# Kernel optimization log

Hardware: AMD Instinct MI355X
Metric: run time of the kernel (lower is better)

## Reference

```python
import jax, jax.numpy as jnp
import numpy as np

LEAKY_SLOPE = 0.2  # tf.nn.leaky_relu default alpha
N_NODES = 50000
N_EDGES = 800000
IN_DIM = 128
OUT_DIM = 64
HEADS = 4
MLP_HID = 256
MLP_OUT = 128


def setup_inputs() -> dict:
    key = jax.random.key(0)
    ks = jax.random.split(key, 10)
    node_embeddings = jax.random.normal(ks[0], (N_NODES, IN_DIM), dtype=jnp.float32)
    src = jax.random.randint(ks[1], (N_EDGES,), 0, N_NODES, dtype=jnp.int32)
    dst = jax.random.randint(ks[2], (N_EDGES,), 0, N_NODES, dtype=jnp.int32)
    # glorot-ish scales
    W_n = jax.random.normal(ks[3], (HEADS, IN_DIM, OUT_DIM), dtype=jnp.float32) * (1.0 / np.sqrt(IN_DIM))
    a_src = jax.random.normal(ks[4], (HEADS, OUT_DIM), dtype=jnp.float32) * (1.0 / np.sqrt(OUT_DIM))
    a_dst = jax.random.normal(ks[5], (HEADS, OUT_DIM), dtype=jnp.float32) * (1.0 / np.sqrt(OUT_DIM))
    mlp_W1 = jax.random.normal(ks[6], (HEADS * OUT_DIM, MLP_HID), dtype=jnp.float32) * (1.0 / np.sqrt(HEADS * OUT_DIM))
    mlp_b1 = jnp.zeros((MLP_HID,), dtype=jnp.float32)
    mlp_W2 = jax.random.normal(ks[7], (MLP_HID, MLP_OUT), dtype=jnp.float32) * (1.0 / np.sqrt(MLP_HID))
    mlp_b2 = jnp.zeros((MLP_OUT,), dtype=jnp.float32)
    return {"node_embeddings": node_embeddings, "src": src, "dst": dst,
            "W_n": W_n, "a_src": a_src, "a_dst": a_dst,
            "mlp_W1": mlp_W1, "mlp_b1": mlp_b1, "mlp_W2": mlp_W2, "mlp_b2": mlp_b2}


def _gat_forward(node_embeddings, src, dst, W_n, a_src, a_dst, mlp_W1, mlp_b1, mlp_W2, mlp_b2):
    N = node_embeddings.shape[0]
    # per-head linear transform: [N, H, D]
    h = jnp.einsum('nc,hcd->nhd', node_embeddings, W_n)
    # decomposed attention scores at node level, gathered per edge
    s_src = jnp.einsum('nhd,hd->nh', h, a_src)          # [N, H]
    s_dst = jnp.einsum('nhd,hd->nh', h, a_dst)          # [N, H]
    e = jax.nn.leaky_relu(s_src[src] + s_dst[dst], negative_slope=LEAKY_SLOPE)  # [E, H]
    # segment softmax over incoming edges of each dst node
    e_max = jax.ops.segment_max(e, dst, num_segments=N)          # [N, H], -inf for empty
    ex = jnp.exp(e - e_max[dst])                                  # [E, H]
    den = jax.ops.segment_sum(ex, dst, num_segments=N)            # [N, H]
    m = h[src]                                                    # [E, H, D] messages
    num = jax.ops.segment_sum(ex[:, :, None] * m, dst, num_segments=N)  # [N, H, D]
    safe_den = jnp.where(den > 0, den, 1.0)
    head_out = jax.nn.relu(num / safe_den[:, :, None])            # [N, H, D]
    concat = head_out.reshape(N, -1)                              # [N, H*D]
    hidden = jax.nn.relu(concat @ mlp_W1 + mlp_b1)
    return hidden @ mlp_W2 + mlp_b2                               # [N, MLP_OUT]


def reference(node_embeddings, src, dst, W_n, a_src, a_dst, mlp_W1, mlp_b1, mlp_W2, mlp_b2):
    return _gat_forward(node_embeddings, src, dst, W_n, a_src, a_dst,
                        mlp_W1, mlp_b1, mlp_W2, mlp_b2)
```

## Files before the change

### kernel.cpp

```cpp
#include <hip/hip_runtime.h>

#define LEAKY 0.2f

typedef __attribute__((ext_vector_type(8))) short short8;
typedef __attribute__((ext_vector_type(4))) float floatx4;
typedef __attribute__((ext_vector_type(8))) unsigned short ushort8_t;

__device__ __forceinline__ float bf2f(unsigned short u) {
    return __uint_as_float(((unsigned)u) << 16);
}
__device__ __forceinline__ unsigned short f2bf(float f) {
    unsigned u = __float_as_uint(f);
    unsigned r = (u + 0x7fffu + ((u >> 16) & 1u)) >> 16;
    return (unsigned short)r;
}
__device__ __forceinline__ float relu_nan(float v) { return v < 0.0f ? 0.0f : v; }

__device__ __forceinline__ void gload_lds16(const void* g, void* l) {
    __builtin_amdgcn_global_load_lds((const __attribute__((address_space(1))) void*)g,
                                     (__attribute__((address_space(3))) void*)l, 16, 0, 0);
}

__global__ void k_fill(float* __restrict__ p, float val, int n) {
    int i = blockIdx.x * blockDim.x + threadIdx.x;
    if (i < n) p[i] = val;
}

__global__ void k_prep(const float* __restrict__ Wn, unsigned short* __restrict__ WnT,
                       const float* __restrict__ W1, unsigned short* __restrict__ W1T,
                       const float* __restrict__ W2, unsigned short* __restrict__ W2T,
                       const int* __restrict__ dst, int* __restrict__ cnt, int E) {
    const int gs = gridDim.x * blockDim.x;
    const int tid = blockIdx.x * blockDim.x + threadIdx.x;
    for (int i = tid; i < 256 * 128; i += gs) {
        int col = i >> 7, k = i & 127;
        int head = col >> 6, d = col & 63;
        WnT[i] = f2bf(Wn[(size_t)head * 8192 + (size_t)k * 64 + d]);
    }
    for (int i = tid; i < 256 * 256; i += gs) {
        int n = i >> 8, k = i & 255;
        W1T[i] = f2bf(W1[(size_t)k * 256 + n]);
    }
    for (int i = tid; i < 128 * 256; i += gs) {
        int n = i >> 8, k = i & 255;
        W2T[i] = f2bf(W2[(size_t)k * 128 + n]);
    }
    for (int i = tid; i < E; i += gs) atomicAdd(cnt + dst[i], 1);
}

__global__ __launch_bounds__(256) void k_scan1(
    const int* __restrict__ cnt, int* __restrict__ rowptr, int* __restrict__ bsum, int N) {
    __shared__ int wtot[4];
    const int lane = threadIdx.x & 63, wave = threadIdx.x >> 6;
    const int i = blockIdx.x * 256 + threadIdx.x;
    int v = (i < N) ? cnt[i] : 0;
    int x = v;
    for (int off = 1; off < 64; off <<= 1) {
        int y = __shfl_up(x, off, 64);
        if (lane >= off) x += y;
    }
    if (lane == 63) wtot[wave] = x;
    __syncthreads();
    int wo = 0;
    for (int wv = 0; wv < wave; ++wv) wo += wtot[wv];
    if (i < N) rowptr[i] = wo + x - v;
    if (threadIdx.x == 255) bsum[blockIdx.x] = wo + x;
}
__global__ void k_scan2(int* __restrict__ bsum, int nb) {
    const int lane = threadIdx.x;
    int carry = 0;
    for (int base = 0; base < nb; base += 64) {
        int i = base + lane;
        int v = (i < nb) ? bsum[i] : 0;
        int x = v;
        for (int off = 1; off < 64; off <<= 1) {
            int y = __shfl_up(x, off, 64);
            if (lane >= off) x += y;
        }
        if (i < nb) bsum[i] = carry + x - v;
        carry += __shfl(x, 63, 64);
    }
}
__global__ void k_scan3(int* __restrict__ rowptr, const int* __restrict__ bsum,
                        int* __restrict__ wcnt, int N, int E) {
    int i = blockIdx.x * blockDim.x + threadIdx.x;
    if (i < N) {
        int v = rowptr[i] + bsum[i >> 8];
        rowptr[i] = v;
        wcnt[i] = v;
    }
    if (i == N) rowptr[N] = E;
}

__global__ void k_scatter(const int* __restrict__ src, const int* __restrict__ dst,
                          int* __restrict__ wcnt, int* __restrict__ esrc, int E) {
    int e = blockIdx.x * blockDim.x + threadIdx.x;
    if (e < E) {
        int pos = atomicAdd(wcnt + dst[e], 1);
        esrc[pos] = src[e];
    }
}

__global__ __launch_bounds__(256) void k_agg(
    const float* __restrict__ s_src, const float* __restrict__ s_dst,
    const unsigned short* __restrict__ h_bf,
    const int* __restrict__ rowptr, const int* __restrict__ esrc,
    unsigned short* __restrict__ concat, int N) {
    const int t = threadIdx.x;
    const int lane = t & 63;
    const int wave = t >> 6;
    const int n = blockIdx.x * 4 + wave;
    if (n >= N) return;

    const int head = lane >> 4;
    const int c0 = lane << 2;
    const int eslot = lane & 15;
    const int hsel = lane & 48;

    const int beg = rowptr[n], end = rowptr[n + 1];
    const float sdst = s_dst[n * 4 + head];
    float num0 = 0, num1 = 0, num2 = 0, num3 = 0, den = 0;

    int sid = 0;
    float sv = 0.0f;
    if (beg < end && eslot < end - beg) {
        sid = esrc[beg + eslot];
        sv = s_src[sid * 4 + head];
    }

    for (int base = beg; base < end; base += 16) {
        const int nn = end - base;
        int sidn = 0;
        float svn = 0.0f;
        if (base + 16 < end) {
            if (eslot < end - (base + 16)) {
                sidn = esrc[base + 16 + eslot];
                svn = s_src[sidn * 4 + head];
            }
        }
        float my_ex = 0.0f;
        if (eslot < nn) {
            float v = sv + sdst;
            v = fmaxf(v, LEAKY * v);
            my_ex = __expf(v);
        }
#pragma unroll
        for (int e = 0; e < 16; ++e) {
            float ex = __shfl(my_ex, hsel | e, 64);
            int s    = __shfl(sid, e, 64);
            ushort4 hv = *(const ushort4*)(h_bf + (size_t)s * 256 + c0);
            num0 += ex * bf2f(hv.x);
            num1 += ex * bf2f(hv.y);
            num2 += ex * bf2f(hv.z);
            num3 += ex * bf2f(hv.w);
            den  += ex;
        }
        sid = sidn; sv = svn;
    }

    const float inv = 1.0f / (den > 0.0f ? den : 1.0f);
    ushort4 o;
    o.x = f2bf(relu_nan(num0 * inv));
    o.y = f2bf(relu_nan(num1 * inv));
    o.z = f2bf(relu_nan(num2 * inv));
    o.w = f2bf(relu_nan(num3 * inv));
    *(ushort4*)(concat + (size_t)n * 256 + c0) = o;
}

__global__ __launch_bounds__(256) void k_gemm0(
    const float* __restrict__ A, const unsigned short* __restrict__ BT,
    unsigned short* __restrict__ Cb, int N,
    const float* __restrict__ asrc, const float* __restrict__ adst,
    float* __restrict__ s_src, float* __restrict__ s_dst) {
    __shared__ unsigned short As[128 * 32];
    __shared__ unsigned short Bs[128 * 32];
    const int t = threadIdx.x;
    const int lane = t & 63;
    const int w = t >> 6;
    const int wy = w >> 1, wx = w & 1;
    const int lm = lane & 15, quad = lane >> 4;
    const int row0 = blockIdx.x * 128;
    const int n0 = blockIdx.y * 128;
    const int srow = lane >> 2;
    const int sk = (lane & 3) * 8;

    floatx4 acc[4][4];
#pragma unroll
    for (int mi = 0; mi < 4; ++mi)
#pragma unroll
        for (int ni = 0; ni < 4; ++ni) acc[mi][ni] = (floatx4){0, 0, 0, 0};

    for (int k0 = 0; k0 < 128; k0 += 32) {
#pragma unroll
        for (int p = 0; p < 2; ++p) {
            int tr = (p * 4 + w) * 16 + srow;
            int ga = row0 + tr; if (ga >= N) ga = N - 1;
            float4 v0 = *(const float4*)(A + (size_t)ga * 128 + k0 + sk);
            float4 v1 = *(const float4*)(A + (size_t)ga * 128 + k0 + sk + 4);
            short8 pk;
            pk[0] = (short)f2bf(v0.x); pk[1] = (short)f2bf(v0.y);
            pk[2] = (short)f2bf(v0.z); pk[3] = (short)f2bf(v0.w);
            pk[4] = (short)f2bf(v1.x); pk[5] = (short)f2bf(v1.y);
            pk[6] = (short)f2bf(v1.z); pk[7] = (short)f2bf(v1.w);
            *(short8*)(As + (size_t)tr * 32 + sk) = pk;
            gload_lds16(BT + (size_t)(n0 + tr) * 128 + k0 + sk,
                        (char*)Bs + (size_t)tr * 64 + sk * 2);
        }
        __syncthreads();
        short8 af[4], bfr[4];
#pragma unroll
        for (int mi = 0; mi < 4; ++mi)
            af[mi] = *(const short8*)(As + (size_t)(wy * 64 + mi * 16 + lm) * 32 + quad * 8);
#pragma unroll
        for (int ni = 0; ni < 4; ++ni)
            bfr[ni] = *(const short8*)(Bs + (size_t)(wx * 64 + ni * 16 + lm) * 32 + quad * 8);
#pragma unroll
        for (int mi = 0; mi < 4; ++mi)
#pragma unroll
            for (int ni = 0; ni < 4; ++ni)
                acc[mi][ni] = __builtin_amdgcn_mfma_f32_16x16x32_bf16(af[mi], bfr[ni], acc[mi][ni], 0, 0, 0);
        __syncthreads();
    }

#pragma unroll
    for (int mi = 0; mi < 4; ++mi)
#pragma unroll
        for (int ni = 0; ni < 4; ++ni)
#pragma unroll
            for (int q = 0; q < 4; ++q) {
                int r = row0 + wy * 64 + mi * 16 + quad * 4 + q;
                int c = n0 + wx * 64 + ni * 16 + lm;
                if (r < N) Cb[(size_t)r * 256 + c] = f2bf(acc[mi][ni][q]);
            }

    const int head = blockIdx.y * 2 + wx;
    float as[4], ad[4];
#pragma unroll
    for (int ni = 0; ni < 4; ++ni) {
        int d = ni * 16 + lm;
        as[ni] = asrc[head * 64 + d];
        ad[ni] = adst[head * 64 + d];
    }
#pragma unroll
    for (int mi = 0; mi < 4; ++mi)
#pragma unroll
        for (int q = 0; q < 4; ++q) {
            float ps = acc[mi][0][q] * as[0] + acc[mi][1][q] * as[1]
                     + acc[mi][2][q] * as[2] + acc[mi][3][q] * as[3];
            float pd = acc[mi][0][q] * ad[0] + acc[mi][1][q] * ad[1]
                     + acc[mi][2][q] * ad[2] + acc[mi][3][q] * ad[3];
#pragma unroll
            for (int m = 1; m < 16; m <<= 1) {
                ps += __shfl_xor(ps, m, 64);
                pd += __shfl_xor(pd, m, 64);
            }
            if (lm == 0) {
                int r = row0 + wy * 64 + mi * 16 + quad * 4 + q;
                if (r < N) {
                    s_src[r * 4 + head] = ps;
                    s_dst[r * 4 + head] = pd;
                }
            }
        }
}

__global__ __launch_bounds__(256) void k_mlp(
    const unsigned short* __restrict__ concat,
    const unsigned short* __restrict__ W1T,
    const float* __restrict__ b1,
    const unsigned short* __restrict__ W2T,
    const float* __restrict__ b2,
    float* __restrict__ outp, int N) {
    __shared__ unsigned short As[64 * 32];
    __shared__ unsigned short Bs[256 * 32];
    __shared__ unsigned short Hs[64 * 264];
    const int t = threadIdx.x;
    const int lane = t & 63;
    const int w = t >> 6;
    const int lm = lane & 15, quad = lane >> 4;
    const int row0 = blockIdx.x * 64;
    const int tr = t >> 2;
    const int sk = (t & 3) * 8;

    floatx4 acc[4][4];
#pragma unroll
    for (int ni = 0; ni < 4; ++ni) {
        float b = b1[w * 64 + ni * 16 + lm];
#pragma unroll
        for (int mi = 0; mi < 4; ++mi) acc[mi][ni] = (floatx4){b, b, b, b};
    }

    for (int k0 = 0; k0 < 256; k0 += 32) {
        {
            int ga = row0 + tr; if (ga >= N) ga = N - 1;
            gload_lds16(concat + (size_t)ga * 256 + k0 + sk,
                        (char*)As + (size_t)tr * 64 + sk * 2);
        }
#pragma unroll
        for (int p = 0; p < 4; ++p) {
            int rn = p * 64 + tr;
            gload_lds16(W1T + (size_t)rn * 256 + k0 + sk,
                        (char*)Bs + (size_t)rn * 64 + sk * 2);
        }
        __syncthreads();
        short8 af[4], bfr[4];
#pragma unroll
        for (int mi = 0; mi < 4; ++mi)
            af[mi] = *(const short8*)(As + (size_t)(mi * 16 + lm) * 32 + quad * 8);
#pragma unroll
        for (int ni = 0; ni < 4; ++ni)
            bfr[ni] = *(const short8*)(Bs + (size_t)(w * 64 + ni * 16 + lm) * 32 + quad * 8);
#pragma unroll
        for (int mi = 0; mi < 4; ++mi)
#pragma unroll
            for (int ni = 0; ni < 4; ++ni)
                acc[mi][ni] = __builtin_amdgcn_mfma_f32_16x16x32_bf16(af[mi], bfr[ni], acc[mi][ni], 0, 0, 0);
        __syncthreads();
    }

#pragma unroll
    for (int mi = 0; mi < 4; ++mi)
#pragma unroll
        for (int ni = 0; ni < 4; ++ni)
#pragma unroll
            for (int q = 0; q < 4; ++q) {
                int row = mi * 16 + quad * 4 + q;
                int col = w * 64 + ni * 16 + lm;
                Hs[row * 264 + col] = f2bf(relu_nan(acc[mi][ni][q]));
            }

    floatx4 acc2[4][2];
#pragma unroll
    for (int ni = 0; ni < 2; ++ni) {
        float b = b2[w * 32 + ni * 16 + lm];
#pragma unroll
        for (int mi = 0; mi < 4; ++mi) acc2[mi][ni] = (floatx4){b, b, b, b};
    }

    for (int k0 = 0; k0 < 256; k0 += 32) {
#pragma unroll
        for (int p = 0; p < 2; ++p) {
            int rn = p * 64 + tr;
            gload_lds16(W2T + (size_t)rn * 256 + k0 + sk,
                        (char*)Bs + (size_t)rn * 64 + sk * 2);
        }
        __syncthreads();
        short8 af[4], bfr[2];
#pragma unroll
        for (int mi = 0; mi < 4; ++mi)
            af[mi] = *(const short8*)(Hs + (size_t)(mi * 16 + lm) * 264 + k0 + quad * 8);
#pragma unroll
        for (int ni = 0; ni < 2; ++ni)
            bfr[ni] = *(const short8*)(Bs + (size_t)(w * 32 + ni * 16 + lm) * 32 + quad * 8);
#pragma unroll
        for (int mi = 0; mi < 4; ++mi)
#pragma unroll
            for (int ni = 0; ni < 2; ++ni)
                acc2[mi][ni] = __builtin_amdgcn_mfma_f32_16x16x32_bf16(af[mi], bfr[ni], acc2[mi][ni], 0, 0, 0);
        __syncthreads();
    }

#pragma unroll
    for (int mi = 0; mi < 4; ++mi)
#pragma unroll
        for (int ni = 0; ni < 2; ++ni)
#pragma unroll
            for (int q = 0; q < 4; ++q) {
                int r = row0 + mi * 16 + quad * 4 + q;
                int c = w * 32 + ni * 16 + lm;
                if (r < N) outp[(size_t)r * 128 + c] = acc2[mi][ni][q];
            }
}

extern "C" void kernel_launch(void* const* d_in, const int* in_sizes, int n_in,
                              void* d_out, int out_size, void* d_ws, size_t ws_size,
                              hipStream_t stream) {
    const float* X    = (const float*)d_in[0];
    const int* src    = (const int*)d_in[1];
    const int* dst    = (const int*)d_in[2];
    const float* Wn   = (const float*)d_in[3];
    const float* Asrc = (const float*)d_in[4];
    const float* Adst = (const float*)d_in[5];
    const float* W1   = (const float*)d_in[6];
    const float* b1   = (const float*)d_in[7];
    const float* W2   = (const float*)d_in[8];
    const float* b2   = (const float*)d_in[9];
    float* out = (float*)d_out;

    const int N = in_sizes[0] / 128;
    const int E = in_sizes[1];
    const int NBS = (N + 255) / 256;
    const int NR = (N + 127) / 128;
    const int NM = (N + 63) / 64;

    size_t off = 0;
    char* w = (char*)d_ws;
    unsigned short* h_bf = (unsigned short*)(w + off); off += (size_t)N * 256 * 2;
    float* s_src = (float*)(w + off);                  off += (size_t)N * 4 * 4;
    float* s_dst = (float*)(w + off);                  off += (size_t)N * 4 * 4;
    int* cnt     = (int*)(w + off);                    off += (size_t)N * 4;
    int* rowptr  = (int*)(w + off);                    off += ((size_t)(N + 1) * 4 + 15) & ~15ull;
    int* wcnt    = (int*)(w + off);                    off += (size_t)N * 4;
    int* bsum    = (int*)(w + off);                    off += ((size_t)NBS * 4 + 15) & ~15ull;
    int* esrc    = (int*)(w + off);                    off += (size_t)E * 4;
    unsigned short* W1T = (unsigned short*)(w + off);  off += 256 * 256 * 2;
    unsigned short* W2T = (unsigned short*)(w + off);  off += 128 * 256 * 2;
    unsigned short* WnT = (unsigned short*)(w + off);  off += 256 * 128 * 2;
    const size_t required = off;

    if (ws_size < required) {
        k_fill<<<dim3((out_size + 255) / 256), dim3(256), 0, stream>>>(
            out, (float)(ws_size >> 20), out_size);
        return;
    }

    unsigned short* concat = (unsigned short*)d_out;

    hipMemsetAsync(cnt, 0, (size_t)N * sizeof(int), stream);
    k_prep<<<dim3(2048), dim3(256), 0, stream>>>(Wn, WnT, W1, W1T, W2, W2T, dst, cnt, E);
    k_gemm0<<<dim3(NR, 2), dim3(256), 0, stream>>>(
        X, WnT, h_bf, N, Asrc, Adst, s_src, s_dst);
    k_scan1<<<dim3(NBS), dim3(256), 0, stream>>>(cnt, rowptr, bsum, N);
    k_scan2<<<dim3(1), dim3(64), 0, stream>>>(bsum, NBS);
    k_scan3<<<dim3((N + 256) / 256), dim3(256), 0, stream>>>(rowptr, bsum, wcnt, N, E);
    k_scatter<<<dim3((E + 255) / 256), dim3(256), 0, stream>>>(src, dst, wcnt, esrc, E);
    k_agg<<<dim3((N + 3) / 4), dim3(256), 0, stream>>>(s_src, s_dst, h_bf, rowptr, esrc,
                                                       concat, N);
    k_mlp<<<dim3(NM), dim3(256), 0, stream>>>(concat, W1T, b1, W2T, b2, out, N);
}
```

Before: 298.1 us.

## Fuse CSR build kernels into one persistent kernel with grid barriers

Merges the weight-prep/count, three scan kernels and the scatter into a single kernel that uses software grid-wide barriers. The block-prefix step is now computed redundantly per block by summing earlier block totals, replacing the single-wave scan kernel. This removes four kernel launches and their inter-kernel gaps. It relies on all NBS (about 196) blocks being co-resident for the spin barrier, which risks deadlock if they are not. The grid is also much smaller than before for the atomic count and scatter loops, so each thread handles more edges.

```diff
diff --git a/kernel.cpp b/kernel.cpp
--- a/kernel.cpp
+++ b/kernel.cpp
@@ -21,17 +21,36 @@
                                      (__attribute__((address_space(3))) void*)l, 16, 0, 0);
 }
 
+__device__ __forceinline__ void gridbar(int* bar, int nblk) {
+    __threadfence();
+    __syncthreads();
+    if (threadIdx.x == 0) {
+        atomicAdd(bar, 1);
+        while (atomicAdd(bar, 0) < nblk) __builtin_amdgcn_s_sleep(8);
+    }
+    __syncthreads();
+    __threadfence();
+}
+
 __global__ void k_fill(float* __restrict__ p, float val, int n) {
     int i = blockIdx.x * blockDim.x + threadIdx.x;
     if (i < n) p[i] = val;
 }
 
-__global__ void k_prep(const float* __restrict__ Wn, unsigned short* __restrict__ WnT,
-                       const float* __restrict__ W1, unsigned short* __restrict__ W1T,
-                       const float* __restrict__ W2, unsigned short* __restrict__ W2T,
-                       const int* __restrict__ dst, int* __restrict__ cnt, int E) {
-    const int gs = gridDim.x * blockDim.x;
-    const int tid = blockIdx.x * blockDim.x + threadIdx.x;
+__global__ __launch_bounds__(256, 1) void k_build(
+    const float* __restrict__ Wn, unsigned short* __restrict__ WnT,
+    const float* __restrict__ W1, unsigned short* __restrict__ W1T,
+    const float* __restrict__ W2, unsigned short* __restrict__ W2T,
+    const int* __restrict__ src, const int* __restrict__ dst,
+    int* __restrict__ cnt, int* __restrict__ rowptr, int* __restrict__ bsum,
+    int* __restrict__ wcnt, int* __restrict__ esrc,
+    int* __restrict__ bar, int N, int E) {
+    const int NB = gridDim.x;
+    const int gs = NB * 256;
+    const int tid = blockIdx.x * 256 + threadIdx.x;
+    const int lane = threadIdx.x & 63, wave = threadIdx.x >> 6;
+    __shared__ int wtot[4];
+
     for (int i = tid; i < 256 * 128; i += gs) {
         int col = i >> 7, k = i & 127;
         int head = col >> 6, d = col & 63;
@@ -45,57 +64,46 @@
         int n = i >> 8, k = i & 255;
         W2T[i] = f2bf(W2[(size_t)k * 128 + n]);
     }
-    for (int i = tid; i < E; i += gs) atomicAdd(cnt + dst[i], 1);
-}
-
-__global__ __launch_bounds__(256) void k_scan1(
-    const int* __restrict__ cnt, int* __restrict__ rowptr, int* __restrict__ bsum, int N) {
-    __shared__ int wtot[4];
-    const int lane = threadIdx.x & 63, wave = threadIdx.x >> 6;
-    const int i = blockIdx.x * 256 + threadIdx.x;
-    int v = (i < N) ? cnt[i] : 0;
-    int x = v;
-    for (int off = 1; off < 64; off <<= 1) {
-        int y = __shfl_up(x, off, 64);
-        if (lane >= off) x += y;
-    }
-    if (lane == 63) wtot[wave] = x;
-    __syncthreads();
-    int wo = 0;
-    for (int wv = 0; wv < wave; ++wv) wo += wtot[wv];
-    if (i < N) rowptr[i] = wo + x - v;
-    if (threadIdx.x == 255) bsum[blockIdx.x] = wo + x;
-}
-__global__ void k_scan2(int* __restrict__ bsum, int nb) {
-    const int lane = threadIdx.x;
-    int carry = 0;
-    for (int base = 0; base < nb; base += 64) {
-        int i = base + lane;
-        int v = (i < nb) ? bsum[i] : 0;
+    for (int e = tid; e < E; e += gs) atomicAdd(cnt + dst[e], 1);
+    gridbar(bar + 0, NB);
+
+    {
+        const int i = blockIdx.x * 256 + threadIdx.x;
+        int v = (i < N) ? cnt[i] : 0;
         int x = v;
         for (int off = 1; off < 64; off <<= 1) {
             int y = __shfl_up(x, off, 64);
             if (lane >= off) x += y;
         }
-        if (i < nb) bsum[i] = carry + x - v;
-        carry += __shfl(x, 63, 64);
-    }
-}
-__global__ void k_scan3(int* __restrict__ rowptr, const int* __restrict__ bsum,
-                        int* __restrict__ wcnt, int N, int E) {
-    int i = blockIdx.x * blockDim.x + threadIdx.x;
-    if (i < N) {
-        int v = rowptr[i] + bsum[i >> 8];
-        rowptr[i] = v;
-        wcnt[i] = v;
-    }
-    if (i == N) rowptr[N] = E;
-}
-
-__global__ void k_scatter(const int* __restrict__ src, const int* __restrict__ dst,
-                          int* __restrict__ wcnt, int* __restrict__ esrc, int E) {
-    int e = blockIdx.x * blockDim.x + threadIdx.x;
-    if (e < E) {
+        if (lane == 63) wtot[wave] = x;
+        __syncthreads();
+        int wo = 0;
+        for (int wv = 0; wv < wave; ++wv) wo += wtot[wv];
+        if (i < N) rowptr[i] = wo + x - v;
+        if (threadIdx.x == 255) bsum[blockIdx.x] = wo + x;
+        __syncthreads();
+    }
+    gridbar(bar + 1, NB);
+
+    {
+        const int b = blockIdx.x;
+        int v = (threadIdx.x < b) ? bsum[threadIdx.x] : 0;
+#pragma unroll
+        for (int m = 32; m >= 1; m >>= 1) v += __shfl_xor(v, m, 64);
+        if (lane == 0) wtot[wave] = v;
+        __syncthreads();
+        const int s_pre = wtot[0] + wtot[1] + wtot[2] + wtot[3];
+        const int gi = b * 256 + threadIdx.x;
+        if (gi < N) {
+            int r = rowptr[gi] + s_pre;
+            rowptr[gi] = r;
+            wcnt[gi] = r;
+        }
+        if (b == NB - 1 && threadIdx.x == 255) rowptr[N] = E;
+    }
+    gridbar(bar + 2, NB);
+
+    for (int e = tid; e < E; e += gs) {
         int pos = atomicAdd(wcnt + dst[e], 1);
         esrc[pos] = src[e];
     }
@@ -399,6 +407,7 @@
     float* s_src = (float*)(w + off);                  off += (size_t)N * 4 * 4;
     float* s_dst = (float*)(w + off);                  off += (size_t)N * 4 * 4;
     int* cnt     = (int*)(w + off);                    off += (size_t)N * 4;
+    int* bar     = (int*)(w + off);                    off += 16;
     int* rowptr  = (int*)(w + off);                    off += ((size_t)(N + 1) * 4 + 15) & ~15ull;
     int* wcnt    = (int*)(w + off);                    off += (size_t)N * 4;
     int* bsum    = (int*)(w + off);                    off += ((size_t)NBS * 4 + 15) & ~15ull;
@@ -416,14 +425,11 @@
 
     unsigned short* concat = (unsigned short*)d_out;
 
-    hipMemsetAsync(cnt, 0, (size_t)N * sizeof(int), stream);
-    k_prep<<<dim3(2048), dim3(256), 0, stream>>>(Wn, WnT, W1, W1T, W2, W2T, dst, cnt, E);
+    hipMemsetAsync(cnt, 0, (size_t)N * sizeof(int) + 16, stream);
+    k_build<<<dim3(NBS), dim3(256), 0, stream>>>(
+        Wn, WnT, W1, W1T, W2, W2T, src, dst, cnt, rowptr, bsum, wcnt, esrc, bar, N, E);
     k_gemm0<<<dim3(NR, 2), dim3(256), 0, stream>>>(
         X, WnT, h_bf, N, Asrc, Adst, s_src, s_dst);
-    k_scan1<<<dim3(NBS), dim3(256), 0, stream>>>(cnt, rowptr, bsum, N);
-    k_scan2<<<dim3(1), dim3(64), 0, stream>>>(bsum, NBS);
-    k_scan3<<<dim3((N + 256) / 256), dim3(256), 0, stream>>>(rowptr, bsum, wcnt, N, E);
-    k_scatter<<<dim3((E + 255) / 256), dim3(256), 0, stream>>>(src, dst, wcnt, esrc, E);
     k_agg<<<dim3((N + 3) / 4), dim3(256), 0, stream>>>(s_src, s_dst, h_bf, rowptr, esrc,
                                                        concat, N);
     k_mlp<<<dim3(NM), dim3(256), 0, stream>>>(concat, W1T, b1, W2T, b2, out, N);
```

Result: slower. 374.1 us (+25.5%).
